# Kernel tuning notes

Hardware: AMD Instinct MI355X
Metric: run time of the kernel (lower is better)

Reference implementation:

```python
import jax, jax.numpy as jnp
import numpy as np

GAMMA = 1.4
EX = jnp.array([1.0, 0.0], dtype=jnp.float32)
EY = jnp.array([0.0, 1.0], dtype=jnp.float32)


def _mlp(x, Ws, bs):
    h = x
    for W, b in zip(Ws[:-1], bs[:-1]):
        h = jnp.tanh(h @ W + b)
    return h @ Ws[-1] + bs[-1]


def setup_inputs() -> dict:
    key = jax.random.key(0)
    ks = jax.random.split(key, 24)
    N, NB = 32768, 4096
    inp = {}
    dom = jnp.array([1.5, 1.0], dtype=jnp.float32)
    inp['x_train'] = jax.random.uniform(ks[0], (N, 2), dtype=jnp.float32) * dom
    inp['x_inlet'] = jax.random.uniform(ks[1], (NB, 2), dtype=jnp.float32) * dom
    inp['U_inlet'] = jax.random.normal(ks[2], (NB, 4), dtype=jnp.float32)
    inp['x_base'] = jax.random.uniform(ks[3], (NB, 2), dtype=jnp.float32) * dom
    inp['x_top'] = jax.random.uniform(ks[4], (NB, 2), dtype=jnp.float32) * dom
    inp['x_slipNormal'] = jax.random.uniform(ks[5], (NB, 2), dtype=jnp.float32) * dom
    dims = [2, 128, 128, 128, 128, 4]
    for i in range(5):
        fan_in = dims[i]
        inp[f'W{i}'] = jax.random.normal(ks[6 + i], (dims[i], dims[i + 1]), dtype=jnp.float32) / jnp.sqrt(jnp.float32(fan_in))
        inp[f'b{i}'] = jnp.zeros((dims[i + 1],), dtype=jnp.float32)
    d2 = [2, 64, 64, 1]
    for i in range(3):
        inp[f'V{i}'] = jax.random.normal(ks[12 + i], (d2[i], d2[i + 1]), dtype=jnp.float32) / jnp.sqrt(jnp.float32(d2[i]))
        inp[f'c{i}'] = jnp.zeros((d2[i + 1],), dtype=jnp.float32)
    return inp


def reference(x_train, x_inlet, U_inlet, x_base, x_top, x_slipNormal,
              W0, b0, W1, b1, W2, b2, W3, b3, W4, b4,
              V0, c0, V1, c1, V2, c2):
    Ws = [W0, W1, W2, W3, W4]
    bs = [b0, b1, b2, b3, b4]
    Vs = [V0, V1, V2]
    cs = [c0, c1, c2]

    def fields(xy):
        # per-point: returns [U1..U4, f1..f4, g1..g4] (12,)
        rho, p, u, v = _mlp(xy, Ws, bs)
        E = p / (GAMMA - 1.0) + 0.5 * rho * (u * u + v * v)
        return jnp.stack([
            rho, rho * u, rho * v, E,                               # U
            rho * u, rho * u * u + p, rho * u * v, u * (E + p),     # f (x-flux)
            rho * v, rho * u * v, rho * v * v + p, v * (E + p)])    # g (y-flux)

    def dUx(xy):
        return jax.jvp(fields, (xy,), (EX,))[1][:4]

    def dUy(xy):
        return jax.jvp(fields, (xy,), (EY,))[1][:4]

    def point_residual(xy):
        _, dx = jax.jvp(fields, (xy,), (EX,))   # x-derivs of all 12 fields
        _, dy = jax.jvp(fields, (xy,), (EY,))   # y-derivs
        U_xx = jax.jvp(dUx, (xy,), (EX,))[1]    # second derivs (fwd-over-fwd)
        U_yy = jax.jvp(dUy, (xy,), (EY,))[1]
        mu = 0.01 * _mlp(xy, Vs, cs)[0] ** 2
        res = dx[4:8] + dy[8:12] - mu * (U_xx + U_yy)  # (4,)
        return res, mu

    res, mu = jax.vmap(point_residual)(x_train)  # res: (N,4), mu: (N,)
    physics = jnp.sum(jnp.mean(res ** 2, axis=0))  # r1+r2+r3+r4

    out_in = _mlp(x_inlet, Ws, bs)
    inlet = jnp.sum(jnp.mean((out_in - U_inlet) ** 2, axis=0))

    base = jnp.mean(_mlp(x_base, Ws, bs)[:, 3] ** 2)
    top = jnp.mean(_mlp(x_top, Ws, bs)[:, 3] ** 2)

    ang = -jnp.pi / 18.0
    o = _mlp(x_slipNormal, Ws, bs)
    slip = jnp.mean((-o[:, 2] * jnp.sin(ang) + o[:, 3] * jnp.cos(ang)) ** 2)

    total = physics + 10.0 * (inlet + base + top + slip) + 0.1 * jnp.mean(mu ** 2)
    return total
```

## Files before the change

### kernel.cpp

```cpp
#include <hip/hip_runtime.h>

#define NTRAIN 32768
#define NBDY   4096
#define PHYS_BLOCKS (NTRAIN / 16)
#define BDY_BLOCKS  256

typedef _Float16 f16x8 __attribute__((ext_vector_type(8)));
typedef __fp16   fp16x2 __attribute__((ext_vector_type(2)));
typedef float    f32x4 __attribute__((ext_vector_type(4)));

union FragU { uint4 q; f16x8 b; _Float16 e[8]; };
union F4  { float4 v; float f[4]; };
union U2h { _Float16 e[4]; uint2 d; };
union H2  { fp16x2 h; _Float16 e[2]; unsigned int u; };

__device__ __forceinline__ float fast_tanh(float z) {
    float e = __expf(2.0f * z);
    return 1.0f - 2.0f * __builtin_amdgcn_rcpf(e + 1.0f);
}

__device__ __forceinline__ unsigned int pk2(float a, float b) {
    H2 r; r.h = __builtin_amdgcn_cvt_pkrtz(a, b);
    return r.u;
}

__global__ __launch_bounds__(256) void pack_w_kernel(
    const float* __restrict__ W1, const float* __restrict__ W2,
    const float* __restrict__ W3, const float* __restrict__ V1,
    const float* __restrict__ W4,
    unsigned short* __restrict__ wsU, float* __restrict__ out)
{
    int b = blockIdx.x;
    if (b < 24) {
        int mat = b >> 3, rb = b & 7;
        const float* W = (mat == 0) ? W1 : (mat == 1) ? W2 : W3;
        unsigned int* hiU = (unsigned int*)(wsU + mat * 32768);
        unsigned int* loU = hiU + 8192;
        int n   = threadIdx.x & 127;
        int pr0 = threadIdx.x >> 7;
        #pragma unroll
        for (int it = 0; it < 4; it++) {
            int pr = pr0 + 2 * it;
            int k  = rb * 16 + pr * 2;
            float v0 = W[k * 128 + n];
            float v1 = W[(k + 1) * 128 + n];
            H2 hh, ll;
            hh.e[0] = (_Float16)v0;
            hh.e[1] = (_Float16)v1;
            ll.e[0] = (_Float16)(v0 - (float)hh.e[0]);
            ll.e[1] = (_Float16)(v1 - (float)hh.e[1]);
            int base = ((n >> 4) * 4 + (k >> 5)) * 64 + ((k >> 3) & 3) * 16 + (n & 15);
            int uoff = base * 4 + ((k & 7) >> 1);
            hiU[uoff] = hh.u;
            loU[uoff] = ll.u;
        }
    } else if (b == 24) {
        unsigned int* hiU = (unsigned int*)(wsU + 98304);
        int n   = threadIdx.x & 63;
        int pr0 = threadIdx.x >> 6;
        #pragma unroll
        for (int it = 0; it < 8; it++) {
            int pr = pr0 + 4 * it;
            int k  = pr * 2;
            float v0 = V1[k * 64 + n];
            float v1 = V1[(k + 1) * 64 + n];
            H2 hh;
            hh.e[0] = (_Float16)v0;
            hh.e[1] = (_Float16)v1;
            int base = ((n >> 4) * 2 + (k >> 5)) * 64 + ((k >> 3) & 3) * 16 + (n & 15);
            hiU[base * 4 + ((k & 7) >> 1)] = hh.u;
        }
        if (threadIdx.x == 0) out[0] = 0.f;
    } else {
        _Float16* hi = (_Float16*)(wsU + 102400);
        _Float16* lo = hi + 2048;
        int u4 = threadIdx.x;
        int lane = u4 & 63, ks = u4 >> 6;
        int m  = lane & 15;
        int kb = ks * 32 + ((lane >> 4) << 3);
        FragU fh, fl;
        #pragma unroll
        for (int j = 0; j < 8; j++) {
            float v = (m < 4) ? W4[(kb + j) * 4 + m] : 0.f;
            _Float16 h = (_Float16)v;
            fh.e[j] = h;
            fl.e[j] = (_Float16)(v - (float)h);
        }
        *(uint4*)(hi + u4 * 8) = fh.q;
        *(uint4*)(lo + u4 * 8) = fl.q;
    }
}

__global__ __launch_bounds__(256, 5) void fused_kernel(
    const float* __restrict__ xt,
    const float* __restrict__ x_inlet, const float* __restrict__ U_inlet,
    const float* __restrict__ x_base,  const float* __restrict__ x_top,
    const float* __restrict__ x_slip,
    const float* __restrict__ W0, const float* __restrict__ b0,
    const float* __restrict__ W1, const float* __restrict__ b1,
    const float* __restrict__ W2, const float* __restrict__ b2,
    const float* __restrict__ W3, const float* __restrict__ b3,
    const float* __restrict__ W4, const float* __restrict__ b4,
    const float* __restrict__ V0, const float* __restrict__ c0,
    const float* __restrict__ V1, const float* __restrict__ c1,
    const float* __restrict__ V2, const float* __restrict__ c2,
    const unsigned short* __restrict__ wsU,
    float* __restrict__ out)
{
    __shared__ float SM[5056];
    const int t = threadIdx.x;
    const int wv   = t >> 6;
    const int lane = t & 63;
    const int nn   = lane & 15;
    const int q    = lane >> 4;

    if (blockIdx.x < PHYS_BLOCKS) {
        unsigned short* AhU = (unsigned short*)SM;
        float* OUTF   = SM + 4352;
        float* MUPART = SM + 4608;
        float* BIASF  = SM + 4672;

        const int p = t >> 4;
        const int c = t & 15;

        const int ptIdx = blockIdx.x * 16 + p;
        const float2 xy = *(const float2*)(xt + ptIdx * 2);
        const float x = xy.x, y = xy.y;

        if (t < 128) {
            BIASF[t]       = b1[t];
            BIASF[128 + t] = b2[t];
            BIASF[256 + t] = b3[t];
        }
        {
            const float2 xyn = *(const float2*)(xt + (blockIdx.x * 16 + nn) * 2);
            FragU mb[2];
            #pragma unroll
            for (int ks = 0; ks < 2; ks++) {
                int u0 = ks * 32 + q * 8;
                F4 va0, va1, vb0, vb1, cc0, cc1;
                va0.v = *(const float4*)(V0 + u0);
                va1.v = *(const float4*)(V0 + u0 + 4);
                vb0.v = *(const float4*)(V0 + 64 + u0);
                vb1.v = *(const float4*)(V0 + 64 + u0 + 4);
                cc0.v = *(const float4*)(c0 + u0);
                cc1.v = *(const float4*)(c0 + u0 + 4);
                #pragma unroll
                for (int i = 0; i < 4; i++) {
                    mb[ks].e[i]     = (_Float16)fast_tanh(
                        xyn.x * va0.f[i] + xyn.y * vb0.f[i] + cc0.f[i]);
                    mb[ks].e[4 + i] = (_Float16)fast_tanh(
                        xyn.x * va1.f[i] + xyn.y * vb1.f[i] + cc1.f[i]);
                }
            }
            f32x4 macc = {0.f, 0.f, 0.f, 0.f};
            #pragma unroll
            for (int ks = 0; ks < 2; ks++) {
                FragU vh;
                vh.q = *(const uint4*)(wsU + 98304 + (((wv * 2 + ks) * 64 + lane) << 3));
                macc = __builtin_amdgcn_mfma_f32_16x16x32_f16(vh.b, mb[ks].b, macc, 0, 0, 0);
            }
            int u2 = wv * 16 + q * 4;
            F4 cv, w2;
            cv.v = *(const float4*)(c1 + u2);
            w2.v = *(const float4*)(V2 + u2);
            float partial = 0.f;
            #pragma unroll
            for (int r = 0; r < 4; r++)
                partial += fast_tanh(macc[r] + cv.f[r]) * w2.f[r];
            partial += __shfl_xor(partial, 16);
            partial += __shfl_xor(partial, 32);
            if (lane < 16) MUPART[wv * 16 + nn] = partial;
        }
        {
            float vals[4][8];
            #pragma unroll
            for (int j = 0; j < 8; j++) {
                int u = c * 8 + j;
                float w0 = W0[u], w1 = W0[128 + u];
                float zv = x * w0 + y * w1 + b0[u];
                float tt = fast_tanh(zv);
                float s2 = 1.f - tt * tt;
                float m2 = -2.f * tt * s2;
                vals[0][j] = tt;
                vals[1][j] = s2 * w0;
                vals[2][j] = s2 * w1;
                vals[3][j] = m2 * (w0 * w0 + w1 * w1);
            }
            #pragma unroll
            for (int s = 0; s < 4; s++) {
                uint4 d = make_uint4(pk2(vals[s][0], vals[s][1]),
                                     pk2(vals[s][2], vals[s][3]),
                                     pk2(vals[s][4], vals[s][5]),
                                     pk2(vals[s][6], vals[s][7]));
                *(uint4*)(AhU + (s * 16 + p) * 136 + c * 8) = d;
            }
        }
        __syncthreads();

        #pragma unroll 1
        for (int l = 0; l < 3; l++) {
            const unsigned short* WpL = wsU + l * 32768;
            f32x4 acc[2][4];
            #pragma unroll
            for (int i = 0; i < 2; i++)
                #pragma unroll
                for (int s = 0; s < 4; s++) {
                    acc[i][s][0] = 0.f; acc[i][s][1] = 0.f;
                    acc[i][s][2] = 0.f; acc[i][s][3] = 0.f;
                }
            #pragma unroll
            for (int ks = 0; ks < 4; ks++) {
                FragU bh[4];
                #pragma unroll
                for (int s = 0; s < 4; s++)
                    bh[s].q = *(const uint4*)(AhU + (s * 16 + nn) * 136 + ks * 32 + q * 8);
                FragU wh[2];
                #pragma unroll
                for (int i = 0; i < 2; i++)
                    wh[i].q = *(const uint4*)(WpL + ((((2 * wv + i) * 4 + ks) * 64 + lane) << 3));
                #pragma unroll
                for (int i = 0; i < 2; i++)
                    #pragma unroll
                    for (int s = 0; s < 4; s++)
                        acc[i][s] = __builtin_amdgcn_mfma_f32_16x16x32_f16(
                            wh[i].b, bh[s].b, acc[i][s], 0, 0, 0);
            }
            __syncthreads();
            #pragma unroll
            for (int i = 0; i < 2; i++) {
                int ubase = (2 * wv + i) * 16 + q * 4;
                F4 bv; bv.v = *(const float4*)&BIASF[l * 128 + ubase];
                float vals[4][4];
                #pragma unroll
                for (int r = 0; r < 4; r++) {
                    float z  = acc[i][0][r] + bv.f[r];
                    float zx = acc[i][1][r], zy = acc[i][2][r];
                    float zl = acc[i][3][r];
                    float tt = fast_tanh(z);
                    float s2 = 1.f - tt * tt;
                    float m2 = -2.f * tt * s2;
                    vals[0][r] = tt;
                    vals[1][r] = s2 * zx;
                    vals[2][r] = s2 * zy;
                    vals[3][r] = s2 * zl + m2 * (zx * zx + zy * zy);
                }
                #pragma unroll
                for (int s = 0; s < 4; s++) {
                    uint2 d = make_uint2(pk2(vals[s][0], vals[s][1]),
                                         pk2(vals[s][2], vals[s][3]));
                    *(uint2*)(AhU + (s * 16 + nn) * 136 + ubase) = d;
                }
            }
            __syncthreads();
        }

        {
            const unsigned short* W4p = wsU + 102400;
            f32x4 a4 = {0.f, 0.f, 0.f, 0.f};
            #pragma unroll
            for (int ks = 0; ks < 4; ks++) {
                FragU bh, wh, wl;
                bh.q = *(const uint4*)(AhU + (wv * 16 + nn) * 136 + ks * 32 + q * 8);
                const unsigned short* base = W4p + ((ks * 64 + lane) << 3);
                wh.q = *(const uint4*)base;
                wl.q = *(const uint4*)(base + 2048);
                a4 = __builtin_amdgcn_mfma_f32_16x16x32_f16(wh.b, bh.b, a4, 0, 0, 0);
                a4 = __builtin_amdgcn_mfma_f32_16x16x32_f16(wl.b, bh.b, a4, 0, 0, 0);
            }
            if (q == 0) {
                float4 o = make_float4(a4[0], a4[1], a4[2], a4[3]);
                if (wv == 0) {
                    o.x += b4[0]; o.y += b4[1]; o.z += b4[2]; o.w += b4[3];
                }
                *(float4*)&OUTF[(wv * 16 + nn) * 4] = o;
            }
        }
        __syncthreads();

        float contrib = 0.f;
        if (t < 16) {
            const int pp = t;
            const float* V   = &OUTF[(0  + pp) * 4];
            const float* DX  = &OUTF[(16 + pp) * 4];
            const float* DY  = &OUTF[(32 + pp) * 4];
            const float* LAP = &OUTF[(48 + pp) * 4];
            float r = V[0],  P = V[1],  u = V[2],  v = V[3];
            float rx = DX[0], Px = DX[1], ux = DX[2], vx = DX[3];
            float ry = DY[0], Py = DY[1], uy = DY[2], vy = DY[3];
            float rl = LAP[0], Pl = LAP[1], ul = LAP[2], vl = LAP[3];
            const float GI = 2.5f;

            float s = MUPART[pp] + MUPART[16 + pp] + MUPART[32 + pp]
                    + MUPART[48 + pp] + c2[0];
            float mu = 0.01f * s * s;

            float q2 = u * u + v * v;
            float E  = P * GI + 0.5f * r * q2;
            float Ex = Px * GI + 0.5f * rx * q2 + r * (u * ux + v * vx);
            float Ey = Py * GI + 0.5f * ry * q2 + r * (u * uy + v * vy);
            float EpP = E + P;

            float f1x = rx * u + r * ux;
            float f2x = rx * u * u + 2.f * r * u * ux + Px;
            float f3x = rx * u * v + r * ux * v + r * u * vx;
            float f4x = ux * EpP + u * (Ex + Px);

            float g1y = ry * v + r * vy;
            float g2y = ry * u * v + r * uy * v + r * u * vy;
            float g3y = ry * v * v + 2.f * r * v * vy + Py;
            float g4y = vy * EpP + v * (Ey + Py);

            float qx  = 2.f * (u * ux + v * vx);
            float qy  = 2.f * (u * uy + v * vy);
            float ql  = 2.f * (ux * ux + uy * uy + vx * vx + vy * vy)
                      + 2.f * (u * ul + v * vl);

            float U1s = rl;
            float U2s = rl * u + 2.f * (rx * ux + ry * uy) + r * ul;
            float U3s = rl * v + 2.f * (rx * vx + ry * vy) + r * vl;
            float U4s = Pl * GI
                      + 0.5f * (rl * q2 + 2.f * (rx * qx + ry * qy) + r * ql);

            float r1 = f1x + g1y - mu * U1s;
            float r2 = f2x + g2y - mu * U2s;
            float r3 = f3x + g3y - mu * U3s;
            float r4 = f4x + g4y - mu * U4s;

            contrib = (r1 * r1 + r2 * r2 + r3 * r3 + r4 * r4 + 0.1f * mu * mu)
                      * (1.0f / (float)NTRAIN);
        }
        if (t < 64) {
            contrib += __shfl_down(contrib, 32);
            contrib += __shfl_down(contrib, 16);
            contrib += __shfl_down(contrib, 8);
            contrib += __shfl_down(contrib, 4);
            contrib += __shfl_down(contrib, 2);
            contrib += __shfl_down(contrib, 1);
            if (t == 0) atomicAdd(out, contrib);
        }
    } else {
        unsigned short* ShU = (unsigned short*)SM;
        float* OUTB  = SM + 4352;
        float* BIASB = SM + 4608;

        const int bb    = blockIdx.x - PHYS_BLOCKS;
        const int batch = bb >> 6;
        const int lb    = bb & 63;
        const float* xs = (batch == 0) ? x_inlet
                        : (batch == 1) ? x_base
                        : (batch == 2) ? x_top : x_slip;
        const int base_pt = lb * 64;

        {
            int p2 = t & 63, ug = t >> 6;
            float2 xy = *(const float2*)(xs + (base_pt + p2) * 2);
            float x = xy.x, y = xy.y;
            #pragma unroll
            for (int g = 0; g < 8; g++) {
                int u0 = ug * 32 + g * 4;
                F4 wa, wb, bbv;
                wa.v  = *(const float4*)(W0 + u0);
                wb.v  = *(const float4*)(W0 + 128 + u0);
                bbv.v = *(const float4*)(b0 + u0);
                float t0 = fast_tanh(x * wa.f[0] + y * wb.f[0] + bbv.f[0]);
                float t1 = fast_tanh(x * wa.f[1] + y * wb.f[1] + bbv.f[1]);
                float t2 = fast_tanh(x * wa.f[2] + y * wb.f[2] + bbv.f[2]);
                float t3 = fast_tanh(x * wa.f[3] + y * wb.f[3] + bbv.f[3]);
                uint2 d = make_uint2(pk2(t0, t1), pk2(t2, t3));
                *(uint2*)(ShU + p2 * 136 + u0) = d;
            }
            if (t < 128) {
                BIASB[t]       = b1[t];
                BIASB[128 + t] = b2[t];
                BIASB[256 + t] = b3[t];
            }
        }
        __syncthreads();

        #pragma unroll 1
        for (int l = 0; l < 3; l++) {
            const unsigned short* WpL = wsU + l * 32768;
            f32x4 acc[2][4];
            #pragma unroll
            for (int i = 0; i < 2; i++)
                #pragma unroll
                for (int n = 0; n < 4; n++) {
                    acc[i][n][0] = 0.f; acc[i][n][1] = 0.f;
                    acc[i][n][2] = 0.f; acc[i][n][3] = 0.f;
                }
            #pragma unroll
            for (int ks = 0; ks < 4; ks++) {
                FragU bh[4];
                #pragma unroll
                for (int n = 0; n < 4; n++)
                    bh[n].q = *(const uint4*)(ShU + (n * 16 + nn) * 136 + ks * 32 + q * 8);
                FragU wh[2];
                #pragma unroll
                for (int i = 0; i < 2; i++)
                    wh[i].q = *(const uint4*)(WpL + ((((2 * wv + i) * 4 + ks) * 64 + lane) << 3));
                #pragma unroll
                for (int i = 0; i < 2; i++)
                    #pragma unroll
                    for (int n = 0; n < 4; n++)
                        acc[i][n] = __builtin_amdgcn_mfma_f32_16x16x32_f16(
                            wh[i].b, bh[n].b, acc[i][n], 0, 0, 0);
            }
            __syncthreads();
            #pragma unroll
            for (int i = 0; i < 2; i++) {
                int ubase = (2 * wv + i) * 16 + q * 4;
                F4 bv; bv.v = *(const float4*)&BIASB[l * 128 + ubase];
                #pragma unroll
                for (int n = 0; n < 4; n++) {
                    float t0 = fast_tanh(acc[i][n][0] + bv.f[0]);
                    float t1 = fast_tanh(acc[i][n][1] + bv.f[1]);
                    float t2 = fast_tanh(acc[i][n][2] + bv.f[2]);
                    float t3 = fast_tanh(acc[i][n][3] + bv.f[3]);
                    uint2 d = make_uint2(pk2(t0, t1), pk2(t2, t3));
                    *(uint2*)(ShU + (n * 16 + nn) * 136 + ubase) = d;
                }
            }
            __syncthreads();
        }

        {
            const unsigned short* W4p = wsU + 102400;
            f32x4 a4 = {0.f, 0.f, 0.f, 0.f};
            #pragma unroll
            for (int ks = 0; ks < 4; ks++) {
                FragU bh, wh, wl;
                bh.q = *(const uint4*)(ShU + (wv * 16 + nn) * 136 + ks * 32 + q * 8);
                const unsigned short* base = W4p + ((ks * 64 + lane) << 3);
                wh.q = *(const uint4*)base;
                wl.q = *(const uint4*)(base + 2048);
                a4 = __builtin_amdgcn_mfma_f32_16x16x32_f16(wh.b, bh.b, a4, 0, 0, 0);
                a4 = __builtin_amdgcn_mfma_f32_16x16x32_f16(wl.b, bh.b, a4, 0, 0, 0);
            }
            if (q == 0) {
                float4 o = make_float4(a4[0] + b4[0], a4[1] + b4[1],
                                       a4[2] + b4[2], a4[3] + b4[3]);
                *(float4*)&OUTB[(wv * 16 + nn) * 4] = o;
            }
        }
        __syncthreads();

        float contrib = 0.f;
        if (t < 64) {
            float o0 = OUTB[t * 4 + 0], o1 = OUTB[t * 4 + 1];
            float o2 = OUTB[t * 4 + 2], o3 = OUTB[t * 4 + 3];
            float l;
            if (batch == 0) {
                float4 Ui = *(const float4*)(U_inlet + (base_pt + t) * 4);
                float d0 = o0 - Ui.x, d1 = o1 - Ui.y, d2 = o2 - Ui.z, d3 = o3 - Ui.w;
                l = d0 * d0 + d1 * d1 + d2 * d2 + d3 * d3;
            } else if (batch == 3) {
                const float sa = -0.17364817766693033f;
                const float ca =  0.9848077530122080f;
                float d = -o2 * sa + o3 * ca;
                l = d * d;
            } else {
                l = o3 * o3;
            }
            contrib = 10.0f * l * (1.0f / (float)NBDY);
        }
        if (t < 64) {
            contrib += __shfl_down(contrib, 32);
            contrib += __shfl_down(contrib, 16);
            contrib += __shfl_down(contrib, 8);
            contrib += __shfl_down(contrib, 4);
            contrib += __shfl_down(contrib, 2);
            contrib += __shfl_down(contrib, 1);
            if (t == 0) atomicAdd(out, contrib);
        }
    }
}

extern "C" void kernel_launch(void* const* d_in, const int* in_sizes, int n_in,
                              void* d_out, int out_size, void* d_ws, size_t ws_size,
                              hipStream_t stream) {
    const float* xt      = (const float*)d_in[0];
    const float* x_inlet = (const float*)d_in[1];
    const float* U_inlet = (const float*)d_in[2];
    const float* x_base  = (const float*)d_in[3];
    const float* x_top   = (const float*)d_in[4];
    const float* x_slip  = (const float*)d_in[5];
    const float* W0 = (const float*)d_in[6];
    const float* b0 = (const float*)d_in[7];
    const float* W1 = (const float*)d_in[8];
    const float* b1 = (const float*)d_in[9];
    const float* W2 = (const float*)d_in[10];
    const float* b2 = (const float*)d_in[11];
    const float* W3 = (const float*)d_in[12];
    const float* b3 = (const float*)d_in[13];
    const float* W4 = (const float*)d_in[14];
    const float* b4 = (const float*)d_in[15];
    const float* V0 = (const float*)d_in[16];
    const float* c0 = (const float*)d_in[17];
    const float* V1 = (const float*)d_in[18];
    const float* c1 = (const float*)d_in[19];
    const float* V2 = (const float*)d_in[20];
    const float* c2 = (const float*)d_in[21];
    float* out = (float*)d_out;
    unsigned short* wsU = (unsigned short*)d_ws;

    pack_w_kernel<<<26, 256, 0, stream>>>(W1, W2, W3, V1, W4, wsU, out);

    fused_kernel<<<PHYS_BLOCKS + BDY_BLOCKS, 256, 0, stream>>>(
        xt, x_inlet, U_inlet, x_base, x_top, x_slip,
        W0, b0, W1, b1, W2, b2, W3, b3, W4, b4,
        V0, c0, V1, c1, V2, c2, wsU, out);
}
```

Measured before the change: 135.6 us.

## Process 32 training points per block to double weight-fragment reuse

Each physics block now handles 32 collocation points instead of 16, so every weight fragment loaded from global memory feeds twice as many MFMAs across 8 row tiles. The mu-network, first layer, hidden-layer epilogue, output layer and residual stage are all re-indexed for two point groups, and shared memory grows to hold the larger activation tile. In exchange the kernel needs more accumulator registers and LDS, occupancy drops from 5 to 4 blocks per CU, and half as many physics blocks are launched.

```diff
diff --git a/kernel.cpp b/kernel.cpp
--- a/kernel.cpp
+++ b/kernel.cpp
@@ -2,7 +2,7 @@
 
 #define NTRAIN 32768
 #define NBDY   4096
-#define PHYS_BLOCKS (NTRAIN / 16)
+#define PHYS_BLOCKS (NTRAIN / 32)
 #define BDY_BLOCKS  256
 
 typedef _Float16 f16x8 __attribute__((ext_vector_type(8)));
@@ -91,7 +91,7 @@
     }
 }
 
-__global__ __launch_bounds__(256, 5) void fused_kernel(
+__global__ __launch_bounds__(256, 4) void fused_kernel(
     const float* __restrict__ xt,
     const float* __restrict__ x_inlet, const float* __restrict__ U_inlet,
     const float* __restrict__ x_base,  const float* __restrict__ x_top,
@@ -107,7 +107,7 @@
     const unsigned short* __restrict__ wsU,
     float* __restrict__ out)
 {
-    __shared__ float SM[5056];
+    __shared__ float SM[9664];
     const int t = threadIdx.x;
     const int wv   = t >> 6;
     const int lane = t & 63;
@@ -116,24 +116,19 @@
 
     if (blockIdx.x < PHYS_BLOCKS) {
         unsigned short* AhU = (unsigned short*)SM;
-        float* OUTF   = SM + 4352;
-        float* MUPART = SM + 4608;
-        float* BIASF  = SM + 4672;
-
-        const int p = t >> 4;
-        const int c = t & 15;
-
-        const int ptIdx = blockIdx.x * 16 + p;
-        const float2 xy = *(const float2*)(xt + ptIdx * 2);
-        const float x = xy.x, y = xy.y;
+        float* OUTF   = SM + 8704;
+        float* MUPART = SM + 9216;
+        float* BIASF  = SM + 9280;
 
         if (t < 128) {
             BIASF[t]       = b1[t];
             BIASF[128 + t] = b2[t];
             BIASF[256 + t] = b3[t];
         }
+
         {
-            const float2 xyn = *(const float2*)(xt + (blockIdx.x * 16 + nn) * 2);
+            const int g = wv >> 1, h = wv & 1;
+            const float2 xyn = *(const float2*)(xt + (blockIdx.x * 32 + g * 16 + nn) * 2);
             FragU mb[2];
             #pragma unroll
             for (int ks = 0; ks < 2; ks++) {
@@ -153,47 +148,58 @@
                         xyn.x * va1.f[i] + xyn.y * vb1.f[i] + cc1.f[i]);
                 }
             }
-            f32x4 macc = {0.f, 0.f, 0.f, 0.f};
-            #pragma unroll
-            for (int ks = 0; ks < 2; ks++) {
-                FragU vh;
-                vh.q = *(const uint4*)(wsU + 98304 + (((wv * 2 + ks) * 64 + lane) << 3));
-                macc = __builtin_amdgcn_mfma_f32_16x16x32_f16(vh.b, mb[ks].b, macc, 0, 0, 0);
-            }
-            int u2 = wv * 16 + q * 4;
-            F4 cv, w2;
-            cv.v = *(const float4*)(c1 + u2);
-            w2.v = *(const float4*)(V2 + u2);
             float partial = 0.f;
             #pragma unroll
-            for (int r = 0; r < 4; r++)
-                partial += fast_tanh(macc[r] + cv.f[r]) * w2.f[r];
+            for (int i = 0; i < 2; i++) {
+                f32x4 macc = {0.f, 0.f, 0.f, 0.f};
+                #pragma unroll
+                for (int ks = 0; ks < 2; ks++) {
+                    FragU vh;
+                    vh.q = *(const uint4*)(wsU + 98304 +
+                           ((((2 * h + i) * 2 + ks) * 64 + lane) << 3));
+                    macc = __builtin_amdgcn_mfma_f32_16x16x32_f16(vh.b, mb[ks].b, macc, 0, 0, 0);
+                }
+                int u2 = (2 * h + i) * 16 + q * 4;
+                F4 cv, w2;
+                cv.v = *(const float4*)(c1 + u2);
+                w2.v = *(const float4*)(V2 + u2);
+                #pragma unroll
+                for (int r = 0; r < 4; r++)
+                    partial += fast_tanh(macc[r] + cv.f[r]) * w2.f[r];
+            }
             partial += __shfl_xor(partial, 16);
             partial += __shfl_xor(partial, 32);
             if (lane < 16) MUPART[wv * 16 + nn] = partial;
         }
         {
-            float vals[4][8];
-            #pragma unroll
-            for (int j = 0; j < 8; j++) {
-                int u = c * 8 + j;
-                float w0 = W0[u], w1 = W0[128 + u];
-                float zv = x * w0 + y * w1 + b0[u];
-                float tt = fast_tanh(zv);
-                float s2 = 1.f - tt * tt;
-                float m2 = -2.f * tt * s2;
-                vals[0][j] = tt;
-                vals[1][j] = s2 * w0;
-                vals[2][j] = s2 * w1;
-                vals[3][j] = m2 * (w0 * w0 + w1 * w1);
-            }
-            #pragma unroll
-            for (int s = 0; s < 4; s++) {
-                uint4 d = make_uint4(pk2(vals[s][0], vals[s][1]),
-                                     pk2(vals[s][2], vals[s][3]),
-                                     pk2(vals[s][4], vals[s][5]),
-                                     pk2(vals[s][6], vals[s][7]));
-                *(uint4*)(AhU + (s * 16 + p) * 136 + c * 8) = d;
+            const int pl = t >> 4, c = t & 15;
+            #pragma unroll
+            for (int h = 0; h < 2; h++) {
+                const int p = h * 16 + pl;
+                const float2 xy = *(const float2*)(xt + (blockIdx.x * 32 + p) * 2);
+                const float x = xy.x, y = xy.y;
+                float vals[4][8];
+                #pragma unroll
+                for (int j = 0; j < 8; j++) {
+                    int u = c * 8 + j;
+                    float w0 = W0[u], w1 = W0[128 + u];
+                    float zv = x * w0 + y * w1 + b0[u];
+                    float tt = fast_tanh(zv);
+                    float s2 = 1.f - tt * tt;
+                    float m2 = -2.f * tt * s2;
+                    vals[0][j] = tt;
+                    vals[1][j] = s2 * w0;
+                    vals[2][j] = s2 * w1;
+                    vals[3][j] = m2 * (w0 * w0 + w1 * w1);
+                }
+                #pragma unroll
+                for (int s = 0; s < 4; s++) {
+                    uint4 d = make_uint4(pk2(vals[s][0], vals[s][1]),
+                                         pk2(vals[s][2], vals[s][3]),
+                                         pk2(vals[s][4], vals[s][5]),
+                                         pk2(vals[s][6], vals[s][7]));
+                    *(uint4*)(AhU + ((h * 4 + s) * 16 + pl) * 136 + c * 8) = d;
+                }
             }
         }
         __syncthreads();
@@ -201,55 +207,58 @@
         #pragma unroll 1
         for (int l = 0; l < 3; l++) {
             const unsigned short* WpL = wsU + l * 32768;
-            f32x4 acc[2][4];
+            f32x4 acc[2][8];
             #pragma unroll
             for (int i = 0; i < 2; i++)
                 #pragma unroll
-                for (int s = 0; s < 4; s++) {
+                for (int s = 0; s < 8; s++) {
                     acc[i][s][0] = 0.f; acc[i][s][1] = 0.f;
                     acc[i][s][2] = 0.f; acc[i][s][3] = 0.f;
                 }
             #pragma unroll
             for (int ks = 0; ks < 4; ks++) {
-                FragU bh[4];
-                #pragma unroll
-                for (int s = 0; s < 4; s++)
-                    bh[s].q = *(const uint4*)(AhU + (s * 16 + nn) * 136 + ks * 32 + q * 8);
                 FragU wh[2];
                 #pragma unroll
                 for (int i = 0; i < 2; i++)
                     wh[i].q = *(const uint4*)(WpL + ((((2 * wv + i) * 4 + ks) * 64 + lane) << 3));
                 #pragma unroll
-                for (int i = 0; i < 2; i++)
+                for (int s = 0; s < 8; s++) {
+                    FragU bh;
+                    bh.q = *(const uint4*)(AhU + (s * 16 + nn) * 136 + ks * 32 + q * 8);
+                    acc[0][s] = __builtin_amdgcn_mfma_f32_16x16x32_f16(
+                        wh[0].b, bh.b, acc[0][s], 0, 0, 0);
+                    acc[1][s] = __builtin_amdgcn_mfma_f32_16x16x32_f16(
+                        wh[1].b, bh.b, acc[1][s], 0, 0, 0);
+                }
+            }
+            __syncthreads();
+            #pragma unroll
+            for (int i = 0; i < 2; i++) {
+                const int ubase = (2 * wv + i) * 16 + q * 4;
+                F4 bv; bv.v = *(const float4*)&BIASF[l * 128 + ubase];
+                #pragma unroll
+                for (int g = 0; g < 2; g++) {
+                    float vals[4][4];
                     #pragma unroll
-                    for (int s = 0; s < 4; s++)
-                        acc[i][s] = __builtin_amdgcn_mfma_f32_16x16x32_f16(
-                            wh[i].b, bh[s].b, acc[i][s], 0, 0, 0);
-            }
-            __syncthreads();
-            #pragma unroll
-            for (int i = 0; i < 2; i++) {
-                int ubase = (2 * wv + i) * 16 + q * 4;
-                F4 bv; bv.v = *(const float4*)&BIASF[l * 128 + ubase];
-                float vals[4][4];
-                #pragma unroll
-                for (int r = 0; r < 4; r++) {
-                    float z  = acc[i][0][r] + bv.f[r];
-                    float zx = acc[i][1][r], zy = acc[i][2][r];
-                    float zl = acc[i][3][r];
-                    float tt = fast_tanh(z);
-                    float s2 = 1.f - tt * tt;
-                    float m2 = -2.f * tt * s2;
-                    vals[0][r] = tt;
-                    vals[1][r] = s2 * zx;
-                    vals[2][r] = s2 * zy;
-                    vals[3][r] = s2 * zl + m2 * (zx * zx + zy * zy);
-                }
-                #pragma unroll
-                for (int s = 0; s < 4; s++) {
-                    uint2 d = make_uint2(pk2(vals[s][0], vals[s][1]),
-                                         pk2(vals[s][2], vals[s][3]));
-                    *(uint2*)(AhU + (s * 16 + nn) * 136 + ubase) = d;
+                    for (int r = 0; r < 4; r++) {
+                        float z  = acc[i][g * 4 + 0][r] + bv.f[r];
+                        float zx = acc[i][g * 4 + 1][r];
+                        float zy = acc[i][g * 4 + 2][r];
+                        float zl = acc[i][g * 4 + 3][r];
+                        float tt = fast_tanh(z);
+                        float s2 = 1.f - tt * tt;
+                        float m2 = -2.f * tt * s2;
+                        vals[0][r] = tt;
+                        vals[1][r] = s2 * zx;
+                        vals[2][r] = s2 * zy;
+                        vals[3][r] = s2 * zl + m2 * (zx * zx + zy * zy);
+                    }
+                    #pragma unroll
+                    for (int s = 0; s < 4; s++) {
+                        uint2 d = make_uint2(pk2(vals[s][0], vals[s][1]),
+                                             pk2(vals[s][2], vals[s][3]));
+                        *(uint2*)(AhU + ((g * 4 + s) * 16 + nn) * 136 + ubase) = d;
+                    }
                 }
             }
             __syncthreads();
@@ -257,42 +266,45 @@
 
         {
             const unsigned short* W4p = wsU + 102400;
-            f32x4 a4 = {0.f, 0.f, 0.f, 0.f};
-            #pragma unroll
-            for (int ks = 0; ks < 4; ks++) {
-                FragU bh, wh, wl;
-                bh.q = *(const uint4*)(AhU + (wv * 16 + nn) * 136 + ks * 32 + q * 8);
-                const unsigned short* base = W4p + ((ks * 64 + lane) << 3);
-                wh.q = *(const uint4*)base;
-                wl.q = *(const uint4*)(base + 2048);
-                a4 = __builtin_amdgcn_mfma_f32_16x16x32_f16(wh.b, bh.b, a4, 0, 0, 0);
-                a4 = __builtin_amdgcn_mfma_f32_16x16x32_f16(wl.b, bh.b, a4, 0, 0, 0);
-            }
-            if (q == 0) {
-                float4 o = make_float4(a4[0], a4[1], a4[2], a4[3]);
-                if (wv == 0) {
-                    o.x += b4[0]; o.y += b4[1]; o.z += b4[2]; o.w += b4[3];
-                }
-                *(float4*)&OUTF[(wv * 16 + nn) * 4] = o;
+            #pragma unroll
+            for (int g = 0; g < 2; g++) {
+                const int rt = g * 4 + wv;
+                f32x4 a4 = {0.f, 0.f, 0.f, 0.f};
+                #pragma unroll
+                for (int ks = 0; ks < 4; ks++) {
+                    FragU bh, wh, wl;
+                    bh.q = *(const uint4*)(AhU + (rt * 16 + nn) * 136 + ks * 32 + q * 8);
+                    const unsigned short* base = W4p + ((ks * 64 + lane) << 3);
+                    wh.q = *(const uint4*)base;
+                    wl.q = *(const uint4*)(base + 2048);
+                    a4 = __builtin_amdgcn_mfma_f32_16x16x32_f16(wh.b, bh.b, a4, 0, 0, 0);
+                    a4 = __builtin_amdgcn_mfma_f32_16x16x32_f16(wl.b, bh.b, a4, 0, 0, 0);
+                }
+                if (q == 0) {
+                    float4 o = make_float4(a4[0], a4[1], a4[2], a4[3]);
+                    if (wv == 0) {
+                        o.x += b4[0]; o.y += b4[1]; o.z += b4[2]; o.w += b4[3];
+                    }
+                    *(float4*)&OUTF[(rt * 16 + nn) * 4] = o;
+                }
             }
         }
         __syncthreads();
 
         float contrib = 0.f;
-        if (t < 16) {
-            const int pp = t;
-            const float* V   = &OUTF[(0  + pp) * 4];
-            const float* DX  = &OUTF[(16 + pp) * 4];
-            const float* DY  = &OUTF[(32 + pp) * 4];
-            const float* LAP = &OUTF[(48 + pp) * 4];
+        if (t < 32) {
+            const int pp = t, g = pp >> 4, p15 = pp & 15;
+            const float* V   = &OUTF[((g * 4 + 0) * 16 + p15) * 4];
+            const float* DX  = &OUTF[((g * 4 + 1) * 16 + p15) * 4];
+            const float* DY  = &OUTF[((g * 4 + 2) * 16 + p15) * 4];
+            const float* LAP = &OUTF[((g * 4 + 3) * 16 + p15) * 4];
             float r = V[0],  P = V[1],  u = V[2],  v = V[3];
             float rx = DX[0], Px = DX[1], ux = DX[2], vx = DX[3];
             float ry = DY[0], Py = DY[1], uy = DY[2], vy = DY[3];
             float rl = LAP[0], Pl = LAP[1], ul = LAP[2], vl = LAP[3];
             const float GI = 2.5f;
 
-            float s = MUPART[pp] + MUPART[16 + pp] + MUPART[32 + pp]
-                    + MUPART[48 + pp] + c2[0];
+            float s = MUPART[g * 32 + p15] + MUPART[g * 32 + 16 + p15] + c2[0];
             float mu = 0.01f * s * s;
 
             float q2 = u * u + v * v;
```

Result: faster. 132.8 us (-2.1%).

## Restructure fused kernel to one wave per block, removing block barriers

Applied to the files above, without the earlier changes.

Each block is now a single 64-lane wave that computes all 128 hidden units for its 16 points, instead of four waves splitting units and synchronising via __syncthreads between layers. Biases are read directly from global memory and mu is computed in-wave instead of through shared partials. This removes barrier and LDS staging overhead, but each wave must fetch the full weight set per layer and hold more fragments in registers.

```diff
diff --git a/kernel.cpp b/kernel.cpp
--- a/kernel.cpp
+++ b/kernel.cpp
@@ -2,8 +2,9 @@
 
 #define NTRAIN 32768
 #define NBDY   4096
-#define PHYS_BLOCKS (NTRAIN / 16)
-#define BDY_BLOCKS  256
+#define PHYS_WPROB (NTRAIN / 16)
+#define BDY_WPROB  (4 * NBDY / 64)
+#define LDS_BYTES  (64 * 136 * 2)
 
 typedef _Float16 f16x8 __attribute__((ext_vector_type(8)));
 typedef __fp16   fp16x2 __attribute__((ext_vector_type(2)));
@@ -11,7 +12,6 @@
 
 union FragU { uint4 q; f16x8 b; _Float16 e[8]; };
 union F4  { float4 v; float f[4]; };
-union U2h { _Float16 e[4]; uint2 d; };
 union H2  { fp16x2 h; _Float16 e[2]; unsigned int u; };
 
 __device__ __forceinline__ float fast_tanh(float z) {
@@ -91,7 +91,7 @@
     }
 }
 
-__global__ __launch_bounds__(256, 5) void fused_kernel(
+__global__ __launch_bounds__(64, 3) void fused_kernel(
     const float* __restrict__ xt,
     const float* __restrict__ x_inlet, const float* __restrict__ U_inlet,
     const float* __restrict__ x_base,  const float* __restrict__ x_top,
@@ -107,33 +107,18 @@
     const unsigned short* __restrict__ wsU,
     float* __restrict__ out)
 {
-    __shared__ float SM[5056];
-    const int t = threadIdx.x;
-    const int wv   = t >> 6;
-    const int lane = t & 63;
+    extern __shared__ char SMC[];
+    unsigned short* A = (unsigned short*)SMC;
+    const int lane = threadIdx.x;
     const int nn   = lane & 15;
     const int q    = lane >> 4;
 
-    if (blockIdx.x < PHYS_BLOCKS) {
-        unsigned short* AhU = (unsigned short*)SM;
-        float* OUTF   = SM + 4352;
-        float* MUPART = SM + 4608;
-        float* BIASF  = SM + 4672;
-
-        const int p = t >> 4;
-        const int c = t & 15;
-
-        const int ptIdx = blockIdx.x * 16 + p;
-        const float2 xy = *(const float2*)(xt + ptIdx * 2);
-        const float x = xy.x, y = xy.y;
-
-        if (t < 128) {
-            BIASF[t]       = b1[t];
-            BIASF[128 + t] = b2[t];
-            BIASF[256 + t] = b3[t];
-        }
+    if (blockIdx.x < PHYS_WPROB) {
+        const int pt = blockIdx.x * 16 + nn;
+        const float2 xy = *(const float2*)(xt + pt * 2);
+
+        float mu;
         {
-            const float2 xyn = *(const float2*)(xt + (blockIdx.x * 16 + nn) * 2);
             FragU mb[2];
             #pragma unroll
             for (int ks = 0; ks < 2; ks++) {
@@ -148,37 +133,44 @@
                 #pragma unroll
                 for (int i = 0; i < 4; i++) {
                     mb[ks].e[i]     = (_Float16)fast_tanh(
-                        xyn.x * va0.f[i] + xyn.y * vb0.f[i] + cc0.f[i]);
+                        xy.x * va0.f[i] + xy.y * vb0.f[i] + cc0.f[i]);
                     mb[ks].e[4 + i] = (_Float16)fast_tanh(
-                        xyn.x * va1.f[i] + xyn.y * vb1.f[i] + cc1.f[i]);
-                }
-            }
-            f32x4 macc = {0.f, 0.f, 0.f, 0.f};
-            #pragma unroll
-            for (int ks = 0; ks < 2; ks++) {
-                FragU vh;
-                vh.q = *(const uint4*)(wsU + 98304 + (((wv * 2 + ks) * 64 + lane) << 3));
-                macc = __builtin_amdgcn_mfma_f32_16x16x32_f16(vh.b, mb[ks].b, macc, 0, 0, 0);
-            }
-            int u2 = wv * 16 + q * 4;
-            F4 cv, w2;
-            cv.v = *(const float4*)(c1 + u2);
-            w2.v = *(const float4*)(V2 + u2);
+                        xy.x * va1.f[i] + xy.y * vb1.f[i] + cc1.f[i]);
+                }
+            }
             float partial = 0.f;
             #pragma unroll
-            for (int r = 0; r < 4; r++)
-                partial += fast_tanh(macc[r] + cv.f[r]) * w2.f[r];
+            for (int tu = 0; tu < 4; tu++) {
+                f32x4 macc = {0.f, 0.f, 0.f, 0.f};
+                #pragma unroll
+                for (int ks = 0; ks < 2; ks++) {
+                    FragU vh;
+                    vh.q = *(const uint4*)(wsU + 98304 +
+                           (((tu * 2 + ks) * 64 + lane) << 3));
+                    macc = __builtin_amdgcn_mfma_f32_16x16x32_f16(vh.b, mb[ks].b, macc, 0, 0, 0);
+                }
+                int u2 = tu * 16 + q * 4;
+                F4 cv, w2;
+                cv.v = *(const float4*)(c1 + u2);
+                w2.v = *(const float4*)(V2 + u2);
+                #pragma unroll
+                for (int r = 0; r < 4; r++)
+                    partial += fast_tanh(macc[r] + cv.f[r]) * w2.f[r];
+            }
             partial += __shfl_xor(partial, 16);
             partial += __shfl_xor(partial, 32);
-            if (lane < 16) MUPART[wv * 16 + nn] = partial;
-        }
-        {
+            float s = partial + c2[0];
+            mu = 0.01f * s * s;
+        }
+
+        #pragma unroll
+        for (int j4 = 0; j4 < 4; j4++) {
             float vals[4][8];
             #pragma unroll
             for (int j = 0; j < 8; j++) {
-                int u = c * 8 + j;
+                int u = q * 32 + j4 * 8 + j;
                 float w0 = W0[u], w1 = W0[128 + u];
-                float zv = x * w0 + y * w1 + b0[u];
+                float zv = xy.x * w0 + xy.y * w1 + b0[u];
                 float tt = fast_tanh(zv);
                 float s2 = 1.f - tt * tt;
                 float m2 = -2.f * tt * s2;
@@ -193,50 +185,44 @@
                                      pk2(vals[s][2], vals[s][3]),
                                      pk2(vals[s][4], vals[s][5]),
                                      pk2(vals[s][6], vals[s][7]));
-                *(uint4*)(AhU + (s * 16 + p) * 136 + c * 8) = d;
-            }
-        }
-        __syncthreads();
+                *(uint4*)(A + (s * 16 + nn) * 136 + q * 32 + j4 * 8) = d;
+            }
+        }
 
         #pragma unroll 1
         for (int l = 0; l < 3; l++) {
             const unsigned short* WpL = wsU + l * 32768;
-            f32x4 acc[2][4];
-            #pragma unroll
-            for (int i = 0; i < 2; i++)
+            const float* bl = (l == 0) ? b1 : (l == 1) ? b2 : b3;
+            FragU bf[4][4];
+            #pragma unroll
+            for (int s = 0; s < 4; s++)
+                #pragma unroll
+                for (int ks = 0; ks < 4; ks++)
+                    bf[s][ks].q = *(const uint4*)(A + (s * 16 + nn) * 136 + ks * 32 + q * 8);
+            #pragma unroll
+            for (int ut = 0; ut < 8; ut++) {
+                FragU wh[4];
+                #pragma unroll
+                for (int ks = 0; ks < 4; ks++)
+                    wh[ks].q = *(const uint4*)(WpL + (((ut * 4 + ks) * 64 + lane) << 3));
+                f32x4 acc[4];
                 #pragma unroll
                 for (int s = 0; s < 4; s++) {
-                    acc[i][s][0] = 0.f; acc[i][s][1] = 0.f;
-                    acc[i][s][2] = 0.f; acc[i][s][3] = 0.f;
-                }
-            #pragma unroll
-            for (int ks = 0; ks < 4; ks++) {
-                FragU bh[4];
-                #pragma unroll
-                for (int s = 0; s < 4; s++)
-                    bh[s].q = *(const uint4*)(AhU + (s * 16 + nn) * 136 + ks * 32 + q * 8);
-                FragU wh[2];
-                #pragma unroll
-                for (int i = 0; i < 2; i++)
-                    wh[i].q = *(const uint4*)(WpL + ((((2 * wv + i) * 4 + ks) * 64 + lane) << 3));
-                #pragma unroll
-                for (int i = 0; i < 2; i++)
+                    acc[s][0] = 0.f; acc[s][1] = 0.f;
+                    acc[s][2] = 0.f; acc[s][3] = 0.f;
+                }
+                #pragma unroll
+                for (int ks = 0; ks < 4; ks++)
                     #pragma unroll
                     for (int s = 0; s < 4; s++)
-                        acc[i][s] = __builtin_amdgcn_mfma_f32_16x16x32_f16(
-                            wh[i].b, bh[s].b, acc[i][s], 0, 0, 0);
-            }
-            __syncthreads();
-            #pragma unroll
-            for (int i = 0; i < 2; i++) {
-                int ubase = (2 * wv + i) * 16 + q * 4;
-                F4 bv; bv.v = *(const float4*)&BIASF[l * 128 + ubase];
+                        acc[s] = __builtin_amdgcn_mfma_f32_16x16x32_f16(
+                            wh[ks].b, bf[s][ks].b, acc[s], 0, 0, 0);
+                F4 bv; bv.v = *(const float4*)(bl + ut * 16 + q * 4);
                 float vals[4][4];
                 #pragma unroll
                 for (int r = 0; r < 4; r++) {
-                    float z  = acc[i][0][r] + bv.f[r];
-                    float zx = acc[i][1][r], zy = acc[i][2][r];
-                    float zl = acc[i][3][r];
+                    float z  = acc[0][r] + bv.f[r];
+                    float zx = acc[1][r], zy = acc[2][r], zl = acc[3][r];
                     float tt = fast_tanh(z);
                     float s2 = 1.f - tt * tt;
                     float m2 = -2.f * tt * s2;
@@ -249,51 +235,39 @@
                 for (int s = 0; s < 4; s++) {
                     uint2 d = make_uint2(pk2(vals[s][0], vals[s][1]),
                                          pk2(vals[s][2], vals[s][3]));
-                    *(uint2*)(AhU + (s * 16 + nn) * 136 + ubase) = d;
-                }
-            }
-            __syncthreads();
-        }
-
-        {
-            const unsigned short* W4p = wsU + 102400;
-            f32x4 a4 = {0.f, 0.f, 0.f, 0.f};
-            #pragma unroll
-            for (int ks = 0; ks < 4; ks++) {
-                FragU bh, wh, wl;
-                bh.q = *(const uint4*)(AhU + (wv * 16 + nn) * 136 + ks * 32 + q * 8);
-                const unsigned short* base = W4p + ((ks * 64 + lane) << 3);
-                wh.q = *(const uint4*)base;
-                wl.q = *(const uint4*)(base + 2048);
-                a4 = __builtin_amdgcn_mfma_f32_16x16x32_f16(wh.b, bh.b, a4, 0, 0, 0);
-                a4 = __builtin_amdgcn_mfma_f32_16x16x32_f16(wl.b, bh.b, a4, 0, 0, 0);
-            }
-            if (q == 0) {
-                float4 o = make_float4(a4[0], a4[1], a4[2], a4[3]);
-                if (wv == 0) {
-                    o.x += b4[0]; o.y += b4[1]; o.z += b4[2]; o.w += b4[3];
-                }
-                *(float4*)&OUTF[(wv * 16 + nn) * 4] = o;
-            }
-        }
-        __syncthreads();
+                    *(uint2*)(A + (s * 16 + nn) * 136 + ut * 16 + q * 4) = d;
+                }
+            }
+        }
+
+        f32x4 a4[4];
+        #pragma unroll
+        for (int s = 0; s < 4; s++) {
+            a4[s][0] = 0.f; a4[s][1] = 0.f; a4[s][2] = 0.f; a4[s][3] = 0.f;
+        }
+        #pragma unroll
+        for (int ks = 0; ks < 4; ks++) {
+            FragU wh, wl;
+            const unsigned short* base = wsU + 102400 + ((ks * 64 + lane) << 3);
+            wh.q = *(const uint4*)base;
+            wl.q = *(const uint4*)(base + 2048);
+            #pragma unroll
+            for (int s = 0; s < 4; s++) {
+                FragU bh;
+                bh.q = *(const uint4*)(A + (s * 16 + nn) * 136 + ks * 32 + q * 8);
+                a4[s] = __builtin_amdgcn_mfma_f32_16x16x32_f16(wh.b, bh.b, a4[s], 0, 0, 0);
+                a4[s] = __builtin_amdgcn_mfma_f32_16x16x32_f16(wl.b, bh.b, a4[s], 0, 0, 0);
+            }
+        }
 
         float contrib = 0.f;
-        if (t < 16) {
-            const int pp = t;
-            const float* V   = &OUTF[(0  + pp) * 4];
-            const float* DX  = &OUTF[(16 + pp) * 4];
-            const float* DY  = &OUTF[(32 + pp) * 4];
-            const float* LAP = &OUTF[(48 + pp) * 4];
-            float r = V[0],  P = V[1],  u = V[2],  v = V[3];
-            float rx = DX[0], Px = DX[1], ux = DX[2], vx = DX[3];
-            float ry = DY[0], Py = DY[1], uy = DY[2], vy = DY[3];
-            float rl = LAP[0], Pl = LAP[1], ul = LAP[2], vl = LAP[3];
+        if (q == 0) {
+            float r  = a4[0][0] + b4[0], P = a4[0][1] + b4[1];
+            float u  = a4[0][2] + b4[2], v = a4[0][3] + b4[3];
+            float rx = a4[1][0], Px = a4[1][1], ux = a4[1][2], vx = a4[1][3];
+            float ry = a4[2][0], Py = a4[2][1], uy = a4[2][2], vy = a4[2][3];
+            float rl = a4[3][0], Pl = a4[3][1], ul = a4[3][2], vl = a4[3][3];
             const float GI = 2.5f;
-
-            float s = MUPART[pp] + MUPART[16 + pp] + MUPART[32 + pp]
-                    + MUPART[48 + pp] + c2[0];
-            float mu = 0.01f * s * s;
 
             float q2 = u * u + v * v;
             float E  = P * GI + 0.5f * r * q2;
@@ -330,149 +304,129 @@
             contrib = (r1 * r1 + r2 * r2 + r3 * r3 + r4 * r4 + 0.1f * mu * mu)
                       * (1.0f / (float)NTRAIN);
         }
-        if (t < 64) {
-            contrib += __shfl_down(contrib, 32);
-            contrib += __shfl_down(contrib, 16);
-            contrib += __shfl_down(contrib, 8);
-            contrib += __shfl_down(contrib, 4);
-            contrib += __shfl_down(contrib, 2);
-            contrib += __shfl_down(contrib, 1);
-            if (t == 0) atomicAdd(out, contrib);
-        }
+        contrib += __shfl_down(contrib, 32);
+        contrib += __shfl_down(contrib, 16);
+        contrib += __shfl_down(contrib, 8);
+        contrib += __shfl_down(contrib, 4);
+        contrib += __shfl_down(contrib, 2);
+        contrib += __shfl_down(contrib, 1);
+        if (lane == 0) atomicAdd(out, contrib);
     } else {
-        unsigned short* ShU = (unsigned short*)SM;
-        float* OUTB  = SM + 4352;
-        float* BIASB = SM + 4608;
-
-        const int bb    = blockIdx.x - PHYS_BLOCKS;
-        const int batch = bb >> 6;
-        const int lb    = bb & 63;
+        const int wj    = blockIdx.x - PHYS_WPROB;
+        const int batch = wj >> 6;
+        const int lb    = wj & 63;
         const float* xs = (batch == 0) ? x_inlet
                         : (batch == 1) ? x_base
                         : (batch == 2) ? x_top : x_slip;
         const int base_pt = lb * 64;
 
-        {
-            int p2 = t & 63, ug = t >> 6;
-            float2 xy = *(const float2*)(xs + (base_pt + p2) * 2);
-            float x = xy.x, y = xy.y;
-            #pragma unroll
-            for (int g = 0; g < 8; g++) {
-                int u0 = ug * 32 + g * 4;
-                F4 wa, wb, bbv;
-                wa.v  = *(const float4*)(W0 + u0);
-                wb.v  = *(const float4*)(W0 + 128 + u0);
-                bbv.v = *(const float4*)(b0 + u0);
-                float t0 = fast_tanh(x * wa.f[0] + y * wb.f[0] + bbv.f[0]);
-                float t1 = fast_tanh(x * wa.f[1] + y * wb.f[1] + bbv.f[1]);
-                float t2 = fast_tanh(x * wa.f[2] + y * wb.f[2] + bbv.f[2]);
-                float t3 = fast_tanh(x * wa.f[3] + y * wb.f[3] + bbv.f[3]);
-                uint2 d = make_uint2(pk2(t0, t1), pk2(t2, t3));
-                *(uint2*)(ShU + p2 * 136 + u0) = d;
-            }
-            if (t < 128) {
-                BIASB[t]       = b1[t];
-                BIASB[128 + t] = b2[t];
-                BIASB[256 + t] = b3[t];
-            }
-        }
-        __syncthreads();
+        #pragma unroll 1
+        for (int g2 = 0; g2 < 4; g2++) {
+            const float2 xy = *(const float2*)(xs + (base_pt + g2 * 16 + nn) * 2);
+            #pragma unroll
+            for (int j4 = 0; j4 < 4; j4++) {
+                float tv[8];
+                #pragma unroll
+                for (int j = 0; j < 8; j++) {
+                    int u = q * 32 + j4 * 8 + j;
+                    tv[j] = fast_tanh(xy.x * W0[u] + xy.y * W0[128 + u] + b0[u]);
+                }
+                uint4 d = make_uint4(pk2(tv[0], tv[1]), pk2(tv[2], tv[3]),
+                                     pk2(tv[4], tv[5]), pk2(tv[6], tv[7]));
+                *(uint4*)(A + (g2 * 16 + nn) * 136 + q * 32 + j4 * 8) = d;
+            }
+        }
 
         #pragma unroll 1
         for (int l = 0; l < 3; l++) {
             const unsigned short* WpL = wsU + l * 32768;
-            f32x4 acc[2][4];
-            #pragma unroll
-            for (int i = 0; i < 2; i++)
-                #pragma unroll
-                for (int n = 0; n < 4; n++) {
-                    acc[i][n][0] = 0.f; acc[i][n][1] = 0.f;
-                    acc[i][n][2] = 0.f; acc[i][n][3] = 0.f;
-                }
-            #pragma unroll
-            for (int ks = 0; ks < 4; ks++) {
-                FragU bh[4];
-                #pragma unroll
-                for (int n = 0; n < 4; n++)
-                    bh[n].q = *(const uint4*)(ShU + (n * 16 + nn) * 136 + ks * 32 + q * 8);
-                FragU wh[2];
-                #pragma unroll
-                for (int i = 0; i < 2; i++)
-                    wh[i].q = *(const uint4*)(WpL + ((((2 * wv + i) * 4 + ks) * 64 + lane) << 3));
-                #pragma unroll
-                for (int i = 0; i < 2; i++)
+            const float* bl = (l == 0) ? b1 : (l == 1) ? b2 : b3;
+            FragU bf[4][4];
+            #pragma unroll
+            for (int rt = 0; rt < 4; rt++)
+                #pragma unroll
+                for (int ks = 0; ks < 4; ks++)
+                    bf[rt][ks].q = *(const uint4*)(A + (rt * 16 + nn) * 136 + ks * 32 + q * 8);
+            #pragma unroll
+            for (int ut = 0; ut < 8; ut++) {
+                FragU wh[4];
+                #pragma unroll
+                for (int ks = 0; ks < 4; ks++)
+                    wh[ks].q = *(const uint4*)(WpL + (((ut * 4 + ks) * 64 + lane) << 3));
+                f32x4 acc[4];
+                #pragma unroll
+                for (int rt = 0; rt < 4; rt++) {
+                    acc[rt][0] = 0.f; acc[rt][1] = 0.f;
+                    acc[rt][2] = 0.f; acc[rt][3] = 0.f;
+                }
+                #pragma unroll
+                for (int ks = 0; ks < 4; ks++)
                     #pragma unroll
-                    for (int n = 0; n < 4; n++)
-                        acc[i][n] = __builtin_amdgcn_mfma_f32_16x16x32_f16(
-                            wh[i].b, bh[n].b, acc[i][n], 0, 0, 0);
-            }
-            __syncthreads();
-            #pragma unroll
-            for (int i = 0; i < 2; i++) {
-                int ubase = (2 * wv + i) * 16 + q * 4;
-                F4 bv; bv.v = *(const float4*)&BIASB[l * 128 + ubase];
-                #pragma unroll
-                for (int n = 0; n < 4; n++) {
-                    float t0 = fast_tanh(acc[i][n][0] + bv.f[0]);
-                    float t1 = fast_tanh(acc[i][n][1] + bv.f[1]);
-                    float t2 = fast_tanh(acc[i][n][2] + bv.f[2]);
-                    float t3 = fast_tanh(acc[i][n][3] + bv.f[3]);
+                    for (int rt = 0; rt < 4; rt++)
+                        acc[rt] = __builtin_amdgcn_mfma_f32_16x16x32_f16(
+                            wh[ks].b, bf[rt][ks].b, acc[rt], 0, 0, 0);
+                F4 bv; bv.v = *(const float4*)(bl + ut * 16 + q * 4);
+                #pragma unroll
+                for (int rt = 0; rt < 4; rt++) {
+                    float t0 = fast_tanh(acc[rt][0] + bv.f[0]);
+                    float t1 = fast_tanh(acc[rt][1] + bv.f[1]);
+                    float t2 = fast_tanh(acc[rt][2] + bv.f[2]);
+                    float t3 = fast_tanh(acc[rt][3] + bv.f[3]);
                     uint2 d = make_uint2(pk2(t0, t1), pk2(t2, t3));
-                    *(uint2*)(ShU + (n * 16 + nn) * 136 + ubase) = d;
-                }
-            }
-            __syncthreads();
-        }
-
-        {
-            const unsigned short* W4p = wsU + 102400;
-            f32x4 a4 = {0.f, 0.f, 0.f, 0.f};
-            #pragma unroll
-            for (int ks = 0; ks < 4; ks++) {
-                FragU bh, wh, wl;
-                bh.q = *(const uint4*)(ShU + (wv * 16 + nn) * 136 + ks * 32 + q * 8);
-                const unsigned short* base = W4p + ((ks * 64 + lane) << 3);
-                wh.q = *(const uint4*)base;
-                wl.q = *(const uint4*)(base + 2048);
-                a4 = __builtin_amdgcn_mfma_f32_16x16x32_f16(wh.b, bh.b, a4, 0, 0, 0);
-                a4 = __builtin_amdgcn_mfma_f32_16x16x32_f16(wl.b, bh.b, a4, 0, 0, 0);
-            }
-            if (q == 0) {
-                float4 o = make_float4(a4[0] + b4[0], a4[1] + b4[1],
-                                       a4[2] + b4[2], a4[3] + b4[3]);
-                *(float4*)&OUTB[(wv * 16 + nn) * 4] = o;
-            }
-        }
-        __syncthreads();
+                    *(uint2*)(A + (rt * 16 + nn) * 136 + ut * 16 + q * 4) = d;
+                }
+            }
+        }
+
+        f32x4 a4[4];
+        #pragma unroll
+        for (int rt = 0; rt < 4; rt++) {
+            a4[rt][0] = 0.f; a4[rt][1] = 0.f; a4[rt][2] = 0.f; a4[rt][3] = 0.f;
+        }
+        #pragma unroll
+        for (int ks = 0; ks < 4; ks++) {
+            FragU wh, wl;
+            const unsigned short* base = wsU + 102400 + ((ks * 64 + lane) << 3);
+            wh.q = *(const uint4*)base;
+            wl.q = *(const uint4*)(base + 2048);
+            #pragma unroll
+            for (int rt = 0; rt < 4; rt++) {
+                FragU bh;
+                bh.q = *(const uint4*)(A + (rt * 16 + nn) * 136 + ks * 32 + q * 8);
+                a4[rt] = __builtin_amdgcn_mfma_f32_16x16x32_f16(wh.b, bh.b, a4[rt], 0, 0, 0);
+                a4[rt] = __builtin_amdgcn_mfma_f32_16x16x32_f16(wl.b, bh.b, a4[rt], 0, 0, 0);
+            }
+        }
 
         float contrib = 0.f;
-        if (t < 64) {
-            float o0 = OUTB[t * 4 + 0], o1 = OUTB[t * 4 + 1];
-            float o2 = OUTB[t * 4 + 2], o3 = OUTB[t * 4 + 3];
-            float l;
-            if (batch == 0) {
-                float4 Ui = *(const float4*)(U_inlet + (base_pt + t) * 4);
-                float d0 = o0 - Ui.x, d1 = o1 - Ui.y, d2 = o2 - Ui.z, d3 = o3 - Ui.w;
-                l = d0 * d0 + d1 * d1 + d2 * d2 + d3 * d3;
-            } else if (batch == 3) {
-                const float sa = -0.17364817766693033f;
-                const float ca =  0.9848077530122080f;
-                float d = -o2 * sa + o3 * ca;
-                l = d * d;
-            } else {
-                l = o3 * o3;
-            }
-            contrib = 10.0f * l * (1.0f / (float)NBDY);
-        }
-        if (t < 64) {
-            contrib += __shfl_down(contrib, 32);
-            contrib += __shfl_down(contrib, 16);
-            contrib += __shfl_down(contrib, 8);
-            contrib += __shfl_down(contrib, 4);
-            contrib += __shfl_down(contrib, 2);
-            contrib += __shfl_down(contrib, 1);
-            if (t == 0) atomicAdd(out, contrib);
-        }
+        if (q == 0) {
+            #pragma unroll
+            for (int rt = 0; rt < 4; rt++) {
+                float o0 = a4[rt][0] + b4[0], o1 = a4[rt][1] + b4[1];
+                float o2 = a4[rt][2] + b4[2], o3 = a4[rt][3] + b4[3];
+                float lv;
+                if (batch == 0) {
+                    float4 Ui = *(const float4*)(U_inlet + (base_pt + rt * 16 + nn) * 4);
+                    float d0 = o0 - Ui.x, d1 = o1 - Ui.y, d2 = o2 - Ui.z, d3 = o3 - Ui.w;
+                    lv = d0 * d0 + d1 * d1 + d2 * d2 + d3 * d3;
+                } else if (batch == 3) {
+                    const float sa = -0.17364817766693033f;
+                    const float ca =  0.9848077530122080f;
+                    float d = -o2 * sa + o3 * ca;
+                    lv = d * d;
+                } else {
+                    lv = o3 * o3;
+                }
+                contrib += 10.0f * lv * (1.0f / (float)NBDY);
+            }
+        }
+        contrib += __shfl_down(contrib, 32);
+        contrib += __shfl_down(contrib, 16);
+        contrib += __shfl_down(contrib, 8);
+        contrib += __shfl_down(contrib, 4);
+        contrib += __shfl_down(contrib, 2);
+        contrib += __shfl_down(contrib, 1);
+        if (lane == 0) atomicAdd(out, contrib);
     }
 }
 
@@ -506,7 +460,7 @@
 
     pack_w_kernel<<<26, 256, 0, stream>>>(W1, W2, W3, V1, W4, wsU, out);
 
-    fused_kernel<<<PHYS_BLOCKS + BDY_BLOCKS, 256, 0, stream>>>(
+    fused_kernel<<<PHYS_WPROB + BDY_WPROB, 64, LDS_BYTES, stream>>>(
         xt, x_inlet, U_inlet, x_base, x_top, x_slip,
         W0, b0, W1, b1, W2, b2, W3, b3, W4, b4,
         V0, c0, V1, c1, V2, c2, wsU, out);
```

After: 156.1 us. 1.15x slower.
